# Kernel tuning notes

Hardware: AMD Instinct MI355X
Metric: run time of the kernel (lower is better)

The kernel has to match this reference:

```python
import jax, jax.numpy as jnp
import numpy as np


def _conv1x1(x, w, b):
    # x: (B,C_in,H,W), w: (C_out,C_in), b: (C_out,)
    return jnp.einsum('bchw,oc->bohw', x, w) + b[None, :, None, None]


def _maxpool2x2(x):
    B, C, H, W = x.shape
    return x.reshape(B, C, H // 2, 2, W // 2, 2).max(axis=(3, 5))


def setup_inputs() -> dict:
    key = jax.random.key(0)
    ks = jax.random.split(key, 10)
    B, C, H, W = 16, 64, 64, 64
    d8, d2 = C // 8, C // 2
    s = 0.05
    return {
        'x': jax.random.normal(ks[0], (B, C, H, W), dtype=jnp.float32),
        'w_theta': jax.random.normal(ks[1], (d8, C), dtype=jnp.float32) * s,
        'b_theta': jnp.zeros((d8,), dtype=jnp.float32),
        'w_phi': jax.random.normal(ks[2], (d8, C), dtype=jnp.float32) * s,
        'b_phi': jnp.zeros((d8,), dtype=jnp.float32),
        'w_g': jax.random.normal(ks[3], (d2, C), dtype=jnp.float32) * s,
        'b_g': jnp.zeros((d2,), dtype=jnp.float32),
        'w_o': jax.random.normal(ks[4], (C, d2), dtype=jnp.float32) * s,
        'b_o': jnp.zeros((C,), dtype=jnp.float32),
        'sigma': jnp.ones((1,), dtype=jnp.float32),
    }


def reference(x, w_theta, b_theta, w_phi, b_phi, w_g, b_g, w_o, b_o, sigma):
    B, C, H, W = x.shape
    N = H * W
    theta = _conv1x1(x, w_theta, b_theta).reshape(B, C // 8, N)            # (B, d8, N)
    phi = _maxpool2x2(_conv1x1(x, w_phi, b_phi)).reshape(B, C // 8, N // 4)  # (B, d8, N/4)
    attn = jax.nn.softmax(jnp.einsum('bdn,bdm->bnm', theta, phi), axis=-1)   # (B, N, N/4)
    g = _maxpool2x2(_conv1x1(x, w_g, b_g)).reshape(B, C // 2, N // 4)        # (B, d2, N/4)
    attn_g = jnp.einsum('bcm,bnm->bcn', g, attn).reshape(B, C // 2, H, W)
    attn_g = _conv1x1(attn_g, w_o, b_o)
    return x + sigma[0] * attn_g
```

## Files before the change

### kernel.cpp

```cpp
#include <hip/hip_runtime.h>


#define B_   16
#define C_   64
#define HW_  4096
#define M_   1024

typedef __attribute__((ext_vector_type(8))) short bf16x8;
typedef __attribute__((ext_vector_type(4))) float f32x4;

__device__ __forceinline__ unsigned short f2bf(float f) {
    union { float f; unsigned int u; } v; v.f = f;
    unsigned int r = (v.u + 0x7FFFu + ((v.u >> 16) & 1u)) >> 16;
    return (unsigned short)r;
}
__device__ __forceinline__ unsigned int pack2(float a, float b) {
    return (unsigned int)f2bf(a) | ((unsigned int)f2bf(b) << 16);
}

__global__ __launch_bounds__(256) void proj_kernel(
    const float* __restrict__ x,
    const float* __restrict__ w_theta, const float* __restrict__ b_theta,
    const float* __restrict__ w_phi,   const float* __restrict__ b_phi,
    const float* __restrict__ w_g,     const float* __restrict__ b_g,
    float* __restrict__ theta,
    float* __restrict__ phi_p,
    unsigned short* __restrict__ gT)
{
    __shared__ __align__(16) float x_l[64 * 132];
    __shared__ float pool_l[128][41];

    const int tid = threadIdx.x;
    const int b   = blockIdx.y;
    const int rp  = blockIdx.x;
    const int n0  = rp * 128;

    {
        const float4* src = (const float4*)(x + (size_t)b * C_ * HW_ + n0);
        #pragma unroll
        for (int j = 0; j < 8; j++) {
            int idx = tid + j * 256;
            int c = idx >> 5, p4 = idx & 31;
            float4 v = src[(size_t)c * (HW_ / 4) + p4];
            *(float4*)&x_l[c * 132 + p4 * 4] = v;
        }
    }
    __syncthreads();

    const int px = tid & 127;
    const int og = tid >> 7;

    if (og == 0) {
        float th[8], ph[8], g0[8];
        #pragma unroll
        for (int o = 0; o < 8; o++) { th[o] = b_theta[o]; ph[o] = b_phi[o]; g0[o] = b_g[o]; }
        #pragma unroll 4
        for (int c = 0; c < C_; c++) {
            float xv = x_l[c * 132 + px];
            #pragma unroll
            for (int o = 0; o < 8; o++) th[o] += xv * w_theta[o * 64 + c];
            #pragma unroll
            for (int o = 0; o < 8; o++) ph[o] += xv * w_phi[o * 64 + c];
            #pragma unroll
            for (int o = 0; o < 8; o++) g0[o] += xv * w_g[o * 64 + c];
        }
        float* tout = theta + ((size_t)b * HW_ + n0 + px) * 8;
        ((float4*)tout)[0] = make_float4(th[0], th[1], th[2], th[3]);
        ((float4*)tout)[1] = make_float4(th[4], th[5], th[6], th[7]);
        #pragma unroll
        for (int o = 0; o < 8; o++) { pool_l[px][o] = ph[o]; pool_l[px][8 + o] = g0[o]; }
    } else {
        float gg[24];
        #pragma unroll
        for (int o = 0; o < 24; o++) gg[o] = b_g[8 + o];
        #pragma unroll 4
        for (int c = 0; c < C_; c++) {
            float xv = x_l[c * 132 + px];
            #pragma unroll
            for (int o = 0; o < 24; o++) gg[o] += xv * w_g[(8 + o) * 64 + c];
        }
        #pragma unroll
        for (int o = 0; o < 24; o++) pool_l[px][16 + o] = gg[o];
    }
    __syncthreads();

    if (tid < 32) {
        const int pc  = tid;
        const int p00 = 2 * pc, p01 = 2 * pc + 1, p10 = 64 + 2 * pc, p11 = 65 + 2 * pc;
        const int mq  = rp * 32 + pc;
        float o8[8];
        #pragma unroll
        for (int o = 0; o < 8; o++) {
            o8[o] = fmaxf(fmaxf(pool_l[p00][o], pool_l[p01][o]),
                          fmaxf(pool_l[p10][o], pool_l[p11][o]));
        }
        float* pout = phi_p + ((size_t)b * M_ + mq) * 8;
        ((float4*)pout)[0] = make_float4(o8[0], o8[1], o8[2], o8[3]);
        ((float4*)pout)[1] = make_float4(o8[4], o8[5], o8[6], o8[7]);
    } else if (tid < 64) {
        const int j   = tid - 32;
        const int p00 = 2 * j, p01 = 2 * j + 1, p10 = 64 + 2 * j, p11 = 65 + 2 * j;
        unsigned short* gout = gT + (size_t)b * 32 * M_ + rp * 32 + j;
        #pragma unroll
        for (int c = 0; c < 32; c++) {
            const int s = c + 8;
            float v = fmaxf(fmaxf(pool_l[p00][s], pool_l[p01][s]),
                            fmaxf(pool_l[p10][s], pool_l[p11][s]));
            gout[(size_t)c * M_] = f2bf(v);
        }
    }
}

__global__ __launch_bounds__(256) void attn_kernel(
    const float* __restrict__ x,
    const float* __restrict__ theta,
    const float* __restrict__ phi_p,
    const unsigned short* __restrict__ gT,
    const float* __restrict__ w_o, const float* __restrict__ b_o,
    const float* __restrict__ sigma,
    float* __restrict__ out)
{
    __shared__ __align__(16) float          phi_ch[64 * 8];
    __shared__ __align__(16) unsigned short P_l[64 * 72];
    __shared__ __align__(16) unsigned short gT_l[32 * 72];
    __shared__ float O_l[64 * 33];
    __shared__ float rs_l[64 * 9];

    const int tid   = threadIdx.x;
    const int b     = blockIdx.y;
    const int qbase = blockIdx.x * 64;
    const int lane  = tid & 63;
    const int wv    = tid >> 6;
    const int ln15  = lane & 15;
    const int quad  = lane >> 4;

    const int qg = tid & 31;
    const int mg = tid >> 5;

    float th0[8], th1[8];
    {
        const float* tp = theta + ((size_t)b * HW_ + qbase + qg * 2) * 8;
        float4 a0 = ((const float4*)tp)[0], a1 = ((const float4*)tp)[1];
        float4 a2 = ((const float4*)tp)[2], a3 = ((const float4*)tp)[3];
        th0[0]=a0.x; th0[1]=a0.y; th0[2]=a0.z; th0[3]=a0.w;
        th0[4]=a1.x; th0[5]=a1.y; th0[6]=a1.z; th0[7]=a1.w;
        th1[0]=a2.x; th1[1]=a2.y; th1[2]=a2.z; th1[3]=a2.w;
        th1[4]=a3.x; th1[5]=a3.y; th1[6]=a3.z; th1[7]=a3.w;
    }

    f32x4 acc0 = {0.f, 0.f, 0.f, 0.f};
    f32x4 acc1 = {0.f, 0.f, 0.f, 0.f};
    float rsum0 = 0.f, rsum1 = 0.f;

    for (int ch = 0; ch < 16; ch++) {
        const int m0 = ch * 64;
        __syncthreads();
        if (tid < 128) {
            const float4* src = (const float4*)(phi_p + ((size_t)b * M_ + m0) * 8);
            *(float4*)&phi_ch[tid * 4] = src[tid];
        }
        {
            const int c = tid >> 3, seg = tid & 7;
            const uint4* src = (const uint4*)(gT + ((size_t)b * 32 + c) * M_ + m0 + seg * 8);
            *(uint4*)&gT_l[c * 72 + seg * 8] = *src;
        }
        __syncthreads();

        {
            float pv0[8], pv1[8];
            #pragma unroll
            for (int mi = 0; mi < 8; mi++) {
                const float* ph = &phi_ch[(mg * 8 + mi) * 8];
                float4 pa = *(const float4*)ph;
                float4 pb = *(const float4*)(ph + 4);
                float s0 = th0[0]*pa.x + th0[1]*pa.y + th0[2]*pa.z + th0[3]*pa.w
                         + th0[4]*pb.x + th0[5]*pb.y + th0[6]*pb.z + th0[7]*pb.w;
                float s1 = th1[0]*pa.x + th1[1]*pa.y + th1[2]*pa.z + th1[3]*pa.w
                         + th1[4]*pb.x + th1[5]*pb.y + th1[6]*pb.z + th1[7]*pb.w;
                float p0 = __expf(fminf(s0, 80.f));
                float p1 = __expf(fminf(s1, 80.f));
                rsum0 += p0; rsum1 += p1;
                pv0[mi] = p0; pv1[mi] = p1;
            }
            uint4 w0, w1;
            w0.x = pack2(pv0[0], pv0[1]); w0.y = pack2(pv0[2], pv0[3]);
            w0.z = pack2(pv0[4], pv0[5]); w0.w = pack2(pv0[6], pv0[7]);
            w1.x = pack2(pv1[0], pv1[1]); w1.y = pack2(pv1[2], pv1[3]);
            w1.z = pack2(pv1[4], pv1[5]); w1.w = pack2(pv1[6], pv1[7]);
            *(uint4*)&P_l[(qg * 2)     * 72 + mg * 8] = w0;
            *(uint4*)&P_l[(qg * 2 + 1) * 72 + mg * 8] = w1;
        }
        __syncthreads();

        {
            const int qrow = wv * 16 + ln15;
            #pragma unroll
            for (int sub = 0; sub < 2; sub++) {
                bf16x8 a  = *(const bf16x8*)&P_l[qrow * 72 + sub * 32 + quad * 8];
                bf16x8 b0 = *(const bf16x8*)&gT_l[ln15 * 72 + sub * 32 + quad * 8];
                bf16x8 b1 = *(const bf16x8*)&gT_l[(16 + ln15) * 72 + sub * 32 + quad * 8];
                acc0 = __builtin_amdgcn_mfma_f32_16x16x32_bf16(a, b0, acc0, 0, 0, 0);
                acc1 = __builtin_amdgcn_mfma_f32_16x16x32_bf16(a, b1, acc1, 0, 0, 0);
            }
        }
    }

    rs_l[(qg * 2)     * 9 + mg] = rsum0;
    rs_l[(qg * 2 + 1) * 9 + mg] = rsum1;
    {
        const int qb0 = wv * 16 + quad * 4;
        #pragma unroll
        for (int r = 0; r < 4; r++) {
            O_l[(qb0 + r) * 33 + ln15]      = acc0[r];
            O_l[(qb0 + r) * 33 + 16 + ln15] = acc1[r];
        }
    }
    __syncthreads();

    const int q = tid & 63;
    float rowsum = 0.f;
    #pragma unroll
    for (int k = 0; k < 8; k++) rowsum += rs_l[q * 9 + k];
    const float sg  = sigma[0];
    const float inv = sg / rowsum;
    float o[32];
    #pragma unroll
    for (int c = 0; c < 32; c++) o[c] = O_l[q * 33 + c];
    const size_t xb = (size_t)b * C_ * HW_ + qbase + q;
    #pragma unroll
    for (int k = 0; k < 16; k++) {
        const int co = wv * 16 + k;
        float t = 0.f;
        #pragma unroll
        for (int c = 0; c < 32; c++) t += w_o[co * 32 + c] * o[c];
        out[xb + (size_t)co * HW_] = x[xb + (size_t)co * HW_] + t * inv + sg * b_o[co];
    }
}

extern "C" void kernel_launch(void* const* d_in, const int* in_sizes, int n_in,
                              void* d_out, int out_size, void* d_ws, size_t ws_size,
                              hipStream_t stream)
{
    const float* x       = (const float*)d_in[0];
    const float* w_theta = (const float*)d_in[1];
    const float* b_theta = (const float*)d_in[2];
    const float* w_phi   = (const float*)d_in[3];
    const float* b_phi   = (const float*)d_in[4];
    const float* w_g     = (const float*)d_in[5];
    const float* b_g     = (const float*)d_in[6];
    const float* w_o     = (const float*)d_in[7];
    const float* b_o     = (const float*)d_in[8];
    const float* sigma   = (const float*)d_in[9];
    float* out = (float*)d_out;

    float* theta = (float*)d_ws;
    float* phi_p = theta + (size_t)B_ * HW_ * 8;
    unsigned short* gT = (unsigned short*)(phi_p + (size_t)B_ * M_ * 8);

    proj_kernel<<<dim3(32, B_), 256, 0, stream>>>(
        x, w_theta, b_theta, w_phi, b_phi, w_g, b_g, theta, phi_p, gT);
    attn_kernel<<<dim3(64, B_), 256, 0, stream>>>(
        x, theta, phi_p, gT, w_o, b_o, sigma, out);
}
```

Measured before the change: 155.6 us.

## Compute attention scores with bf16 MFMA and double-buffer phi/g tiles

Theta and pooled phi are now stored as bf16 so the QK^T scores come from MFMA (K=8, zero-padded to 32) instead of scalar FP32 dot products. Each wave keeps its probabilities in its own LDS tile, which removes a block barrier per chunk, and phi/g chunks are double-buffered so the next chunk loads while the current one computes. Row sums are reduced with cross-lane shuffles. The projection kernel reads x straight from global memory instead of staging it in LDS. The trade-off is reduced precision in theta and phi, plus MFMA work wasted on the zero padding.

Measured after the change: 162.2 us. 1.04x slower.

```diff
diff --git a/kernel.cpp b/kernel.cpp
--- a/kernel.cpp
+++ b/kernel.cpp
@@ -11,8 +11,7 @@
 
 __device__ __forceinline__ unsigned short f2bf(float f) {
     union { float f; unsigned int u; } v; v.f = f;
-    unsigned int r = (v.u + 0x7FFFu + ((v.u >> 16) & 1u)) >> 16;
-    return (unsigned short)r;
+    return (unsigned short)((v.u + 0x7FFFu + ((v.u >> 16) & 1u)) >> 16);
 }
 __device__ __forceinline__ unsigned int pack2(float a, float b) {
     return (unsigned int)f2bf(a) | ((unsigned int)f2bf(b) << 16);
@@ -23,61 +22,60 @@
     const float* __restrict__ w_theta, const float* __restrict__ b_theta,
     const float* __restrict__ w_phi,   const float* __restrict__ b_phi,
     const float* __restrict__ w_g,     const float* __restrict__ b_g,
-    float* __restrict__ theta,
-    float* __restrict__ phi_p,
+    unsigned short* __restrict__ thetaB,
+    unsigned short* __restrict__ phiB,
     unsigned short* __restrict__ gT)
 {
-    __shared__ __align__(16) float x_l[64 * 132];
     __shared__ float pool_l[128][41];
-
-    const int tid = threadIdx.x;
-    const int b   = blockIdx.y;
-    const int rp  = blockIdx.x;
-    const int n0  = rp * 128;
-
-    {
-        const float4* src = (const float4*)(x + (size_t)b * C_ * HW_ + n0);
-        #pragma unroll
-        for (int j = 0; j < 8; j++) {
-            int idx = tid + j * 256;
-            int c = idx >> 5, p4 = idx & 31;
-            float4 v = src[(size_t)c * (HW_ / 4) + p4];
-            *(float4*)&x_l[c * 132 + p4 * 4] = v;
-        }
-    }
-    __syncthreads();
-
-    const int px = tid & 127;
-    const int og = tid >> 7;
-
-    if (og == 0) {
+    const int tid  = threadIdx.x;
+    const int b    = blockIdx.y;
+    const int rp   = blockIdx.x;
+    const int n0   = rp * 128;
+    const int px   = tid & 127;
+    const int half = tid >> 7;
+
+    const float* xp = x + (size_t)b * C_ * HW_ + n0 + px;
+
+    if (half == 0) {
         float th[8], ph[8], g0[8];
         #pragma unroll
         for (int o = 0; o < 8; o++) { th[o] = b_theta[o]; ph[o] = b_phi[o]; g0[o] = b_g[o]; }
-        #pragma unroll 4
-        for (int c = 0; c < C_; c++) {
-            float xv = x_l[c * 132 + px];
-            #pragma unroll
-            for (int o = 0; o < 8; o++) th[o] += xv * w_theta[o * 64 + c];
-            #pragma unroll
-            for (int o = 0; o < 8; o++) ph[o] += xv * w_phi[o * 64 + c];
-            #pragma unroll
-            for (int o = 0; o < 8; o++) g0[o] += xv * w_g[o * 64 + c];
-        }
-        float* tout = theta + ((size_t)b * HW_ + n0 + px) * 8;
-        ((float4*)tout)[0] = make_float4(th[0], th[1], th[2], th[3]);
-        ((float4*)tout)[1] = make_float4(th[4], th[5], th[6], th[7]);
+        for (int cg = 0; cg < 4; cg++) {
+            float xv[16];
+            #pragma unroll
+            for (int i = 0; i < 16; i++) xv[i] = xp[(size_t)(cg * 16 + i) * HW_];
+            #pragma unroll
+            for (int i = 0; i < 16; i++) {
+                const int c = cg * 16 + i; const float v = xv[i];
+                #pragma unroll
+                for (int o = 0; o < 8; o++) th[o] += v * w_theta[o * 64 + c];
+                #pragma unroll
+                for (int o = 0; o < 8; o++) ph[o] += v * w_phi[o * 64 + c];
+                #pragma unroll
+                for (int o = 0; o < 8; o++) g0[o] += v * w_g[o * 64 + c];
+            }
+        }
+        unsigned short* tout = thetaB + ((size_t)b * HW_ + n0 + px) * 8;
+        uint4 tv;
+        tv.x = pack2(th[0], th[1]); tv.y = pack2(th[2], th[3]);
+        tv.z = pack2(th[4], th[5]); tv.w = pack2(th[6], th[7]);
+        *(uint4*)tout = tv;
         #pragma unroll
         for (int o = 0; o < 8; o++) { pool_l[px][o] = ph[o]; pool_l[px][8 + o] = g0[o]; }
     } else {
         float gg[24];
         #pragma unroll
         for (int o = 0; o < 24; o++) gg[o] = b_g[8 + o];
-        #pragma unroll 4
-        for (int c = 0; c < C_; c++) {
-            float xv = x_l[c * 132 + px];
-            #pragma unroll
-            for (int o = 0; o < 24; o++) gg[o] += xv * w_g[(8 + o) * 64 + c];
+        for (int cg = 0; cg < 4; cg++) {
+            float xv[16];
+            #pragma unroll
+            for (int i = 0; i < 16; i++) xv[i] = xp[(size_t)(cg * 16 + i) * HW_];
+            #pragma unroll
+            for (int i = 0; i < 16; i++) {
+                const int c = cg * 16 + i; const float v = xv[i];
+                #pragma unroll
+                for (int o = 0; o < 24; o++) gg[o] += v * w_g[(8 + o) * 64 + c];
+            }
         }
         #pragma unroll
         for (int o = 0; o < 24; o++) pool_l[px][16 + o] = gg[o];
@@ -90,13 +88,14 @@
         const int mq  = rp * 32 + pc;
         float o8[8];
         #pragma unroll
-        for (int o = 0; o < 8; o++) {
+        for (int o = 0; o < 8; o++)
             o8[o] = fmaxf(fmaxf(pool_l[p00][o], pool_l[p01][o]),
                           fmaxf(pool_l[p10][o], pool_l[p11][o]));
-        }
-        float* pout = phi_p + ((size_t)b * M_ + mq) * 8;
-        ((float4*)pout)[0] = make_float4(o8[0], o8[1], o8[2], o8[3]);
-        ((float4*)pout)[1] = make_float4(o8[4], o8[5], o8[6], o8[7]);
+        unsigned short* pout = phiB + ((size_t)b * M_ + mq) * 8;
+        uint4 pv;
+        pv.x = pack2(o8[0], o8[1]); pv.y = pack2(o8[2], o8[3]);
+        pv.z = pack2(o8[4], o8[5]); pv.w = pack2(o8[6], o8[7]);
+        *(uint4*)pout = pv;
     } else if (tid < 64) {
         const int j   = tid - 32;
         const int p00 = 2 * j, p01 = 2 * j + 1, p10 = 64 + 2 * j, p11 = 65 + 2 * j;
@@ -113,18 +112,18 @@
 
 __global__ __launch_bounds__(256) void attn_kernel(
     const float* __restrict__ x,
-    const float* __restrict__ theta,
-    const float* __restrict__ phi_p,
-    const unsigned short* __restrict__ gT,
+    const unsigned short* __restrict__ thetaB,
+    const unsigned short* __restrict__ phiB,
+    const unsigned short* __restrict__ gTg,
     const float* __restrict__ w_o, const float* __restrict__ b_o,
     const float* __restrict__ sigma,
     float* __restrict__ out)
 {
-    __shared__ __align__(16) float          phi_ch[64 * 8];
-    __shared__ __align__(16) unsigned short P_l[64 * 72];
-    __shared__ __align__(16) unsigned short gT_l[32 * 72];
+    __shared__ __align__(16) unsigned short pbuf[2][64 * 32];
+    __shared__ __align__(16) unsigned short gbuf[2][32 * 72];
+    __shared__ __align__(16) unsigned short P_buf[4][16 * 72];
     __shared__ float O_l[64 * 33];
-    __shared__ float rs_l[64 * 9];
+    __shared__ float rs_l[64];
 
     const int tid   = threadIdx.x;
     const int b     = blockIdx.y;
@@ -134,79 +133,84 @@
     const int ln15  = lane & 15;
     const int quad  = lane >> 4;
 
-    const int qg = tid & 31;
-    const int mg = tid >> 5;
-
-    float th0[8], th1[8];
+    ((uint4*)pbuf)[tid]       = make_uint4(0, 0, 0, 0);
+    ((uint4*)pbuf)[tid + 256] = make_uint4(0, 0, 0, 0);
+
+    bf16x8 afrag;
     {
-        const float* tp = theta + ((size_t)b * HW_ + qbase + qg * 2) * 8;
-        float4 a0 = ((const float4*)tp)[0], a1 = ((const float4*)tp)[1];
-        float4 a2 = ((const float4*)tp)[2], a3 = ((const float4*)tp)[3];
-        th0[0]=a0.x; th0[1]=a0.y; th0[2]=a0.z; th0[3]=a0.w;
-        th0[4]=a1.x; th0[5]=a1.y; th0[6]=a1.z; th0[7]=a1.w;
-        th1[0]=a2.x; th1[1]=a2.y; th1[2]=a2.z; th1[3]=a2.w;
-        th1[4]=a3.x; th1[5]=a3.y; th1[6]=a3.z; th1[7]=a3.w;
-    }
+        const unsigned short* tp = thetaB + ((size_t)b * HW_ + qbase + wv * 16 + ln15) * 8;
+        afrag = *(const bf16x8*)tp;
+    }
+
+    const int sc  = tid >> 3;
+    const int seg = tid & 7;
 
     f32x4 acc0 = {0.f, 0.f, 0.f, 0.f};
     f32x4 acc1 = {0.f, 0.f, 0.f, 0.f};
-    float rsum0 = 0.f, rsum1 = 0.f;
+    float rs_acc[4] = {0.f, 0.f, 0.f, 0.f};
+
+    __syncthreads();
+
+    {
+        uint4 v = *(const uint4*)(gTg + (((size_t)b * 32 + sc) << 10) + seg * 8);
+        *(uint4*)&gbuf[0][sc * 72 + seg * 8] = v;
+        if (tid < 64) {
+            uint4 p = *(const uint4*)(phiB + ((size_t)b * M_ + tid) * 8);
+            *(uint4*)&pbuf[0][tid * 32] = p;
+        }
+    }
 
     for (int ch = 0; ch < 16; ch++) {
-        const int m0 = ch * 64;
         __syncthreads();
-        if (tid < 128) {
-            const float4* src = (const float4*)(phi_p + ((size_t)b * M_ + m0) * 8);
-            *(float4*)&phi_ch[tid * 4] = src[tid];
-        }
-        {
-            const int c = tid >> 3, seg = tid & 7;
-            const uint4* src = (const uint4*)(gT + ((size_t)b * 32 + c) * M_ + m0 + seg * 8);
-            *(uint4*)&gT_l[c * 72 + seg * 8] = *src;
-        }
-        __syncthreads();
-
-        {
-            float pv0[8], pv1[8];
-            #pragma unroll
-            for (int mi = 0; mi < 8; mi++) {
-                const float* ph = &phi_ch[(mg * 8 + mi) * 8];
-                float4 pa = *(const float4*)ph;
-                float4 pb = *(const float4*)(ph + 4);
-                float s0 = th0[0]*pa.x + th0[1]*pa.y + th0[2]*pa.z + th0[3]*pa.w
-                         + th0[4]*pb.x + th0[5]*pb.y + th0[6]*pb.z + th0[7]*pb.w;
-                float s1 = th1[0]*pa.x + th1[1]*pa.y + th1[2]*pa.z + th1[3]*pa.w
-                         + th1[4]*pb.x + th1[5]*pb.y + th1[6]*pb.z + th1[7]*pb.w;
-                float p0 = __expf(fminf(s0, 80.f));
-                float p1 = __expf(fminf(s1, 80.f));
-                rsum0 += p0; rsum1 += p1;
-                pv0[mi] = p0; pv1[mi] = p1;
-            }
-            uint4 w0, w1;
-            w0.x = pack2(pv0[0], pv0[1]); w0.y = pack2(pv0[2], pv0[3]);
-            w0.z = pack2(pv0[4], pv0[5]); w0.w = pack2(pv0[6], pv0[7]);
-            w1.x = pack2(pv1[0], pv1[1]); w1.y = pack2(pv1[2], pv1[3]);
-            w1.z = pack2(pv1[4], pv1[5]); w1.w = pack2(pv1[6], pv1[7]);
-            *(uint4*)&P_l[(qg * 2)     * 72 + mg * 8] = w0;
-            *(uint4*)&P_l[(qg * 2 + 1) * 72 + mg * 8] = w1;
-        }
-        __syncthreads();
-
-        {
-            const int qrow = wv * 16 + ln15;
-            #pragma unroll
-            for (int sub = 0; sub < 2; sub++) {
-                bf16x8 a  = *(const bf16x8*)&P_l[qrow * 72 + sub * 32 + quad * 8];
-                bf16x8 b0 = *(const bf16x8*)&gT_l[ln15 * 72 + sub * 32 + quad * 8];
-                bf16x8 b1 = *(const bf16x8*)&gT_l[(16 + ln15) * 72 + sub * 32 + quad * 8];
-                acc0 = __builtin_amdgcn_mfma_f32_16x16x32_bf16(a, b0, acc0, 0, 0, 0);
-                acc1 = __builtin_amdgcn_mfma_f32_16x16x32_bf16(a, b1, acc1, 0, 0, 0);
-            }
-        }
-    }
-
-    rs_l[(qg * 2)     * 9 + mg] = rsum0;
-    rs_l[(qg * 2 + 1) * 9 + mg] = rsum1;
+        const int bi = ch & 1;
+        if (ch < 15) {
+            const int m0 = (ch + 1) * 64;
+            uint4 v = *(const uint4*)(gTg + (((size_t)b * 32 + sc) << 10) + m0 + seg * 8);
+            *(uint4*)&gbuf[bi ^ 1][sc * 72 + seg * 8] = v;
+            if (tid < 64) {
+                uint4 p = *(const uint4*)(phiB + ((size_t)b * M_ + m0 + tid) * 8);
+                *(uint4*)&pbuf[bi ^ 1][tid * 32] = p;
+            }
+        }
+
+        const f32x4 zc = {0.f, 0.f, 0.f, 0.f};
+        f32x4 s0 = __builtin_amdgcn_mfma_f32_16x16x32_bf16(
+            afrag, *(const bf16x8*)&pbuf[bi][(0 * 16 + ln15) * 32 + quad * 8], zc, 0, 0, 0);
+        f32x4 s1 = __builtin_amdgcn_mfma_f32_16x16x32_bf16(
+            afrag, *(const bf16x8*)&pbuf[bi][(1 * 16 + ln15) * 32 + quad * 8], zc, 0, 0, 0);
+        f32x4 s2 = __builtin_amdgcn_mfma_f32_16x16x32_bf16(
+            afrag, *(const bf16x8*)&pbuf[bi][(2 * 16 + ln15) * 32 + quad * 8], zc, 0, 0, 0);
+        f32x4 s3 = __builtin_amdgcn_mfma_f32_16x16x32_bf16(
+            afrag, *(const bf16x8*)&pbuf[bi][(3 * 16 + ln15) * 32 + quad * 8], zc, 0, 0, 0);
+
+        #pragma unroll
+        for (int t = 0; t < 4; t++) {
+            f32x4 sv = (t == 0) ? s0 : (t == 1) ? s1 : (t == 2) ? s2 : s3;
+            #pragma unroll
+            for (int r = 0; r < 4; r++) {
+                float p = __expf(fminf(sv[r], 80.f));
+                rs_acc[r] += p;
+                P_buf[wv][(quad * 4 + r) * 72 + t * 16 + ln15] = f2bf(p);
+            }
+        }
+
+        #pragma unroll
+        for (int s_ = 0; s_ < 2; s_++) {
+            bf16x8 pa  = *(const bf16x8*)&P_buf[wv][ln15 * 72 + s_ * 32 + quad * 8];
+            bf16x8 gb0 = *(const bf16x8*)&gbuf[bi][ln15 * 72 + s_ * 32 + quad * 8];
+            bf16x8 gb1 = *(const bf16x8*)&gbuf[bi][(16 + ln15) * 72 + s_ * 32 + quad * 8];
+            acc0 = __builtin_amdgcn_mfma_f32_16x16x32_bf16(pa, gb0, acc0, 0, 0, 0);
+            acc1 = __builtin_amdgcn_mfma_f32_16x16x32_bf16(pa, gb1, acc1, 0, 0, 0);
+        }
+    }
+
+    #pragma unroll
+    for (int r = 0; r < 4; r++) {
+        float v = rs_acc[r];
+        v += __shfl_xor(v, 1); v += __shfl_xor(v, 2);
+        v += __shfl_xor(v, 4); v += __shfl_xor(v, 8);
+        if (ln15 == 0) rs_l[wv * 16 + quad * 4 + r] = v;
+    }
     {
         const int qb0 = wv * 16 + quad * 4;
         #pragma unroll
@@ -218,9 +222,7 @@
     __syncthreads();
 
     const int q = tid & 63;
-    float rowsum = 0.f;
-    #pragma unroll
-    for (int k = 0; k < 8; k++) rowsum += rs_l[q * 9 + k];
+    const float rowsum = rs_l[q];
     const float sg  = sigma[0];
     const float inv = sg / rowsum;
     float o[32];
@@ -253,12 +255,12 @@
     const float* sigma   = (const float*)d_in[9];
     float* out = (float*)d_out;
 
-    float* theta = (float*)d_ws;
-    float* phi_p = theta + (size_t)B_ * HW_ * 8;
-    unsigned short* gT = (unsigned short*)(phi_p + (size_t)B_ * M_ * 8);
+    unsigned short* thetaB = (unsigned short*)d_ws;
+    unsigned short* phiB   = thetaB + (size_t)B_ * HW_ * 8;
+    unsigned short* gT     = phiB + (size_t)B_ * M_ * 8;
 
     proj_kernel<<<dim3(32, B_), 256, 0, stream>>>(
-        x, w_theta, b_theta, w_phi, b_phi, w_g, b_g, theta, phi_p, gT);
+        x, w_theta, b_theta, w_phi, b_phi, w_g, b_g, thetaB, phiB, gT);
     attn_kernel<<<dim3(64, B_), 256, 0, stream>>>(
-        x, theta, phi_p, gT, w_o, b_o, sigma, out);
-}
+        x, thetaB, phiB, gT, w_o, b_o, sigma, out);
+}
```

## Compute attention scores with MFMA and keep P in registers, dropping LDS staging

Applied to the files above, without the earlier changes.

The QK^T score computation moves from scalar FP32 dot products to bf16 MFMA. Phi is zero-padded to a K of 32 and theta is stored as bf16. The MFMA output layout is arranged so the exponentiated scores can be packed straight into B-operand registers for the P·G MFMA, which removes the P and gT shared-memory round trips and the per-chunk __syncthreads. The g columns are permuted in the projection kernel to match that register layout, and the next chunk's operands are software-prefetched from global memory. The cost is bf16 precision for theta and phi, extra zero-padded work in the K dimension, and four times the phi storage.

Result: slower. 159.3 us (+2.4%).

```diff
diff --git a/kernel.cpp b/kernel.cpp
--- a/kernel.cpp
+++ b/kernel.cpp
@@ -11,8 +11,7 @@
 
 __device__ __forceinline__ unsigned short f2bf(float f) {
     union { float f; unsigned int u; } v; v.f = f;
-    unsigned int r = (v.u + 0x7FFFu + ((v.u >> 16) & 1u)) >> 16;
-    return (unsigned short)r;
+    return (unsigned short)((v.u + 0x7FFFu + ((v.u >> 16) & 1u)) >> 16);
 }
 __device__ __forceinline__ unsigned int pack2(float a, float b) {
     return (unsigned int)f2bf(a) | ((unsigned int)f2bf(b) << 16);
@@ -23,9 +22,9 @@
     const float* __restrict__ w_theta, const float* __restrict__ b_theta,
     const float* __restrict__ w_phi,   const float* __restrict__ b_phi,
     const float* __restrict__ w_g,     const float* __restrict__ b_g,
-    float* __restrict__ theta,
-    float* __restrict__ phi_p,
-    unsigned short* __restrict__ gT)
+    unsigned short* __restrict__ thetaB,
+    unsigned short* __restrict__ phiB32,
+    unsigned short* __restrict__ gTp)
 {
     __shared__ __align__(16) float x_l[64 * 132];
     __shared__ float pool_l[128][41];
@@ -64,9 +63,11 @@
             #pragma unroll
             for (int o = 0; o < 8; o++) g0[o] += xv * w_g[o * 64 + c];
         }
-        float* tout = theta + ((size_t)b * HW_ + n0 + px) * 8;
-        ((float4*)tout)[0] = make_float4(th[0], th[1], th[2], th[3]);
-        ((float4*)tout)[1] = make_float4(th[4], th[5], th[6], th[7]);
+        unsigned short* tout = thetaB + ((size_t)b * HW_ + n0 + px) * 8;
+        uint4 tv;
+        tv.x = pack2(th[0], th[1]); tv.y = pack2(th[2], th[3]);
+        tv.z = pack2(th[4], th[5]); tv.w = pack2(th[6], th[7]);
+        *(uint4*)tout = tv;
         #pragma unroll
         for (int o = 0; o < 8; o++) { pool_l[px][o] = ph[o]; pool_l[px][8 + o] = g0[o]; }
     } else {
@@ -90,17 +91,22 @@
         const int mq  = rp * 32 + pc;
         float o8[8];
         #pragma unroll
-        for (int o = 0; o < 8; o++) {
+        for (int o = 0; o < 8; o++)
             o8[o] = fmaxf(fmaxf(pool_l[p00][o], pool_l[p01][o]),
                           fmaxf(pool_l[p10][o], pool_l[p11][o]));
-        }
-        float* pout = phi_p + ((size_t)b * M_ + mq) * 8;
-        ((float4*)pout)[0] = make_float4(o8[0], o8[1], o8[2], o8[3]);
-        ((float4*)pout)[1] = make_float4(o8[4], o8[5], o8[6], o8[7]);
+        unsigned short* pout = phiB32 + ((size_t)b * M_ + mq) * 32;
+        uint4 pv;
+        pv.x = pack2(o8[0], o8[1]); pv.y = pack2(o8[2], o8[3]);
+        pv.z = pack2(o8[4], o8[5]); pv.w = pack2(o8[6], o8[7]);
+        ((uint4*)pout)[0] = pv;
+        ((uint4*)pout)[1] = make_uint4(0, 0, 0, 0);
+        ((uint4*)pout)[2] = make_uint4(0, 0, 0, 0);
+        ((uint4*)pout)[3] = make_uint4(0, 0, 0, 0);
     } else if (tid < 64) {
         const int j   = tid - 32;
         const int p00 = 2 * j, p01 = 2 * j + 1, p10 = 64 + 2 * j, p11 = 65 + 2 * j;
-        unsigned short* gout = gT + (size_t)b * 32 * M_ + rp * 32 + j;
+        const int pcol = rp * 32 + ((j >> 2) & 3) * 8 + (j >> 4) * 4 + (j & 3);
+        unsigned short* gout = gTp + (size_t)b * 32 * M_ + pcol;
         #pragma unroll
         for (int c = 0; c < 32; c++) {
             const int s = c + 8;
@@ -113,114 +119,111 @@
 
 __global__ __launch_bounds__(256) void attn_kernel(
     const float* __restrict__ x,
-    const float* __restrict__ theta,
-    const float* __restrict__ phi_p,
-    const unsigned short* __restrict__ gT,
+    const unsigned short* __restrict__ thetaB,
+    const unsigned short* __restrict__ phiB32,
+    const unsigned short* __restrict__ gTp,
     const float* __restrict__ w_o, const float* __restrict__ b_o,
     const float* __restrict__ sigma,
     float* __restrict__ out)
 {
-    __shared__ __align__(16) float          phi_ch[64 * 8];
-    __shared__ __align__(16) unsigned short P_l[64 * 72];
-    __shared__ __align__(16) unsigned short gT_l[32 * 72];
     __shared__ float O_l[64 * 33];
-    __shared__ float rs_l[64 * 9];
+    __shared__ float rs_l[64];
 
     const int tid   = threadIdx.x;
     const int b     = blockIdx.y;
     const int qbase = blockIdx.x * 64;
+    const int wv    = tid >> 6;
     const int lane  = tid & 63;
-    const int wv    = tid >> 6;
     const int ln15  = lane & 15;
     const int quad  = lane >> 4;
 
-    const int qg = tid & 31;
-    const int mg = tid >> 5;
-
-    float th0[8], th1[8];
-    {
-        const float* tp = theta + ((size_t)b * HW_ + qbase + qg * 2) * 8;
-        float4 a0 = ((const float4*)tp)[0], a1 = ((const float4*)tp)[1];
-        float4 a2 = ((const float4*)tp)[2], a3 = ((const float4*)tp)[3];
-        th0[0]=a0.x; th0[1]=a0.y; th0[2]=a0.z; th0[3]=a0.w;
-        th0[4]=a1.x; th0[5]=a1.y; th0[6]=a1.z; th0[7]=a1.w;
-        th1[0]=a2.x; th1[1]=a2.y; th1[2]=a2.z; th1[3]=a2.w;
-        th1[4]=a3.x; th1[5]=a3.y; th1[6]=a3.z; th1[7]=a3.w;
-    }
+    const unsigned short* phiP = phiB32 + (size_t)b * M_ * 32;
+    const unsigned short* gP   = gTp    + (size_t)b * 32 * M_;
+
+    bf16x8 tfrag;
+    {
+        const unsigned short* tp =
+            thetaB + ((size_t)b * HW_ + qbase + wv * 16 + ln15) * 8;
+        bf16x8 t = *(const bf16x8*)tp;
+        bf16x8 z = {0, 0, 0, 0, 0, 0, 0, 0};
+        tfrag = (quad == 0) ? t : z;
+    }
+
+    #define LD_PHI(ch_, t_) \
+        (*(const bf16x8*)(phiP + ((size_t)((ch_) * 64 + (t_) * 16 + ln15)) * 32 + quad * 8))
+    #define LD_G(ch_, h_, s_) \
+        (*(const bf16x8*)(gP + (size_t)((h_) * 16 + ln15) * M_ + (ch_) * 64 + (s_) * 32 + quad * 8))
 
     f32x4 acc0 = {0.f, 0.f, 0.f, 0.f};
     f32x4 acc1 = {0.f, 0.f, 0.f, 0.f};
-    float rsum0 = 0.f, rsum1 = 0.f;
+    float rs_part = 0.f;
+
+    bf16x8 pf[4], gf[4];
+    #pragma unroll
+    for (int t = 0; t < 4; t++) pf[t] = LD_PHI(0, t);
+    gf[0] = LD_G(0, 0, 0); gf[1] = LD_G(0, 0, 1);
+    gf[2] = LD_G(0, 1, 0); gf[3] = LD_G(0, 1, 1);
 
     for (int ch = 0; ch < 16; ch++) {
-        const int m0 = ch * 64;
-        __syncthreads();
-        if (tid < 128) {
-            const float4* src = (const float4*)(phi_p + ((size_t)b * M_ + m0) * 8);
-            *(float4*)&phi_ch[tid * 4] = src[tid];
-        }
+        const int nc = (ch < 15) ? ch + 1 : 15;
+        bf16x8 npf[4], ngf[4];
+        #pragma unroll
+        for (int t = 0; t < 4; t++) npf[t] = LD_PHI(nc, t);
+        ngf[0] = LD_G(nc, 0, 0); ngf[1] = LD_G(nc, 0, 1);
+        ngf[2] = LD_G(nc, 1, 0); ngf[3] = LD_G(nc, 1, 1);
+
+        const f32x4 zc = {0.f, 0.f, 0.f, 0.f};
+        f32x4 S0 = __builtin_amdgcn_mfma_f32_16x16x32_bf16(pf[0], tfrag, zc, 0, 0, 0);
+        f32x4 S1 = __builtin_amdgcn_mfma_f32_16x16x32_bf16(pf[1], tfrag, zc, 0, 0, 0);
+        f32x4 S2 = __builtin_amdgcn_mfma_f32_16x16x32_bf16(pf[2], tfrag, zc, 0, 0, 0);
+        f32x4 S3 = __builtin_amdgcn_mfma_f32_16x16x32_bf16(pf[3], tfrag, zc, 0, 0, 0);
+
+        union { bf16x8 v; unsigned int u[4]; } pb0, pb1;
         {
-            const int c = tid >> 3, seg = tid & 7;
-            const uint4* src = (const uint4*)(gT + ((size_t)b * 32 + c) * M_ + m0 + seg * 8);
-            *(uint4*)&gT_l[c * 72 + seg * 8] = *src;
-        }
-        __syncthreads();
-
-        {
-            float pv0[8], pv1[8];
-            #pragma unroll
-            for (int mi = 0; mi < 8; mi++) {
-                const float* ph = &phi_ch[(mg * 8 + mi) * 8];
-                float4 pa = *(const float4*)ph;
-                float4 pb = *(const float4*)(ph + 4);
-                float s0 = th0[0]*pa.x + th0[1]*pa.y + th0[2]*pa.z + th0[3]*pa.w
-                         + th0[4]*pb.x + th0[5]*pb.y + th0[6]*pb.z + th0[7]*pb.w;
-                float s1 = th1[0]*pa.x + th1[1]*pa.y + th1[2]*pa.z + th1[3]*pa.w
-                         + th1[4]*pb.x + th1[5]*pb.y + th1[6]*pb.z + th1[7]*pb.w;
-                float p0 = __expf(fminf(s0, 80.f));
-                float p1 = __expf(fminf(s1, 80.f));
-                rsum0 += p0; rsum1 += p1;
-                pv0[mi] = p0; pv1[mi] = p1;
+            float e0[4], e1[4], e2[4], e3[4];
+            #pragma unroll
+            for (int r = 0; r < 4; r++) {
+                e0[r] = __expf(fminf(S0[r], 80.f));
+                e1[r] = __expf(fminf(S1[r], 80.f));
+                e2[r] = __expf(fminf(S2[r], 80.f));
+                e3[r] = __expf(fminf(S3[r], 80.f));
+                rs_part += e0[r] + e1[r] + e2[r] + e3[r];
             }
-            uint4 w0, w1;
-            w0.x = pack2(pv0[0], pv0[1]); w0.y = pack2(pv0[2], pv0[3]);
-            w0.z = pack2(pv0[4], pv0[5]); w0.w = pack2(pv0[6], pv0[7]);
-            w1.x = pack2(pv1[0], pv1[1]); w1.y = pack2(pv1[2], pv1[3]);
-            w1.z = pack2(pv1[4], pv1[5]); w1.w = pack2(pv1[6], pv1[7]);
-            *(uint4*)&P_l[(qg * 2)     * 72 + mg * 8] = w0;
-            *(uint4*)&P_l[(qg * 2 + 1) * 72 + mg * 8] = w1;
-        }
-        __syncthreads();
-
-        {
-            const int qrow = wv * 16 + ln15;
-            #pragma unroll
-            for (int sub = 0; sub < 2; sub++) {
-                bf16x8 a  = *(const bf16x8*)&P_l[qrow * 72 + sub * 32 + quad * 8];
-                bf16x8 b0 = *(const bf16x8*)&gT_l[ln15 * 72 + sub * 32 + quad * 8];
-                bf16x8 b1 = *(const bf16x8*)&gT_l[(16 + ln15) * 72 + sub * 32 + quad * 8];
-                acc0 = __builtin_amdgcn_mfma_f32_16x16x32_bf16(a, b0, acc0, 0, 0, 0);
-                acc1 = __builtin_amdgcn_mfma_f32_16x16x32_bf16(a, b1, acc1, 0, 0, 0);
-            }
-        }
-    }
-
-    rs_l[(qg * 2)     * 9 + mg] = rsum0;
-    rs_l[(qg * 2 + 1) * 9 + mg] = rsum1;
-    {
-        const int qb0 = wv * 16 + quad * 4;
+            pb0.u[0] = pack2(e0[0], e0[1]); pb0.u[1] = pack2(e0[2], e0[3]);
+            pb0.u[2] = pack2(e1[0], e1[1]); pb0.u[3] = pack2(e1[2], e1[3]);
+            pb1.u[0] = pack2(e2[0], e2[1]); pb1.u[1] = pack2(e2[2], e2[3]);
+            pb1.u[2] = pack2(e3[0], e3[1]); pb1.u[3] = pack2(e3[2], e3[3]);
+        }
+
+        acc0 = __builtin_amdgcn_mfma_f32_16x16x32_bf16(gf[0], pb0.v, acc0, 0, 0, 0);
+        acc0 = __builtin_amdgcn_mfma_f32_16x16x32_bf16(gf[1], pb1.v, acc0, 0, 0, 0);
+        acc1 = __builtin_amdgcn_mfma_f32_16x16x32_bf16(gf[2], pb0.v, acc1, 0, 0, 0);
+        acc1 = __builtin_amdgcn_mfma_f32_16x16x32_bf16(gf[3], pb1.v, acc1, 0, 0, 0);
+
+        #pragma unroll
+        for (int t = 0; t < 4; t++) { pf[t] = npf[t]; gf[t] = ngf[t]; }
+    }
+    #undef LD_PHI
+    #undef LD_G
+
+    {
+        float v = rs_part;
+        v += __shfl_xor(v, 16);
+        v += __shfl_xor(v, 32);
+        if (quad == 0) rs_l[wv * 16 + ln15] = v;
+    }
+    {
+        const int q = wv * 16 + ln15;
         #pragma unroll
         for (int r = 0; r < 4; r++) {
-            O_l[(qb0 + r) * 33 + ln15]      = acc0[r];
-            O_l[(qb0 + r) * 33 + 16 + ln15] = acc1[r];
+            O_l[q * 33 + quad * 4 + r]      = acc0[r];
+            O_l[q * 33 + 16 + quad * 4 + r] = acc1[r];
         }
     }
     __syncthreads();
 
     const int q = tid & 63;
-    float rowsum = 0.f;
-    #pragma unroll
-    for (int k = 0; k < 8; k++) rowsum += rs_l[q * 9 + k];
+    const float rowsum = rs_l[q];
     const float sg  = sigma[0];
     const float inv = sg / rowsum;
     float o[32];
@@ -253,12 +256,12 @@
     const float* sigma   = (const float*)d_in[9];
     float* out = (float*)d_out;
 
-    float* theta = (float*)d_ws;
-    float* phi_p = theta + (size_t)B_ * HW_ * 8;
-    unsigned short* gT = (unsigned short*)(phi_p + (size_t)B_ * M_ * 8);
+    unsigned short* thetaB = (unsigned short*)d_ws;
+    unsigned short* phiB32 = thetaB + (size_t)B_ * HW_ * 8;
+    unsigned short* gTp    = phiB32 + (size_t)B_ * M_ * 32;
 
     proj_kernel<<<dim3(32, B_), 256, 0, stream>>>(
-        x, w_theta, b_theta, w_phi, b_phi, w_g, b_g, theta, phi_p, gT);
+        x, w_theta, b_theta, w_phi, b_phi, w_g, b_g, thetaB, phiB32, gTp);
     attn_kernel<<<dim3(64, B_), 256, 0, stream>>>(
-        x, theta, phi_p, gT, w_o, b_o, sigma, out);
-}
+        x, thetaB, phiB32, gTp, w_o, b_o, sigma, out);
+}
```
